# Kernel tuning notes

Measured on AMD Instinct MI355X. Metric: run time of the kernel, lower is better.

## Reference

```python
import jax, jax.numpy as jnp
import numpy as np

N_NODES = 100000
N_EDGES = 1600000
IN_SIZE = 256
HID = 64
HEADS = 2
OUT_SIZE = 16


def _gat_layer(x, W, a_l, a_r, b, src, dst, n_nodes, heads, feat):
    # x: [N, Din]; W: [Din, H*F]; a_l, a_r: [H, F]; b: [H*F]
    h = (x @ W).reshape(n_nodes, heads, feat)          # [N, H, F]
    el = jnp.sum(h * a_l, axis=-1)                     # [N, H]
    er = jnp.sum(h * a_r, axis=-1)                     # [N, H]
    e = jax.nn.leaky_relu(el[src] + er[dst], 0.2)      # [E, H]
    # segment softmax over incoming edges of each dst node
    m = jax.ops.segment_max(e, dst, num_segments=n_nodes)
    m = jnp.where(jnp.isfinite(m), m, 0.0)             # nodes with no in-edges
    p = jnp.exp(e - m[dst])                            # [E, H]
    s = jax.ops.segment_sum(p, dst, num_segments=n_nodes)
    alpha = p / (s[dst] + 1e-9)                        # [E, H]
    # scatter-add weighted source features
    out = jax.ops.segment_sum(alpha[:, :, None] * h[src], dst, num_segments=n_nodes)
    return out + b.reshape(1, heads, feat)             # [N, H, F]


def setup_inputs() -> dict:
    key = jax.random.key(0)
    ks = jax.random.split(key, 12)
    features = jax.random.normal(ks[0], (N_NODES, IN_SIZE), dtype=jnp.float32)
    src = jax.random.randint(ks[1], (N_EDGES,), 0, N_NODES, dtype=jnp.int32)
    dst = jax.random.randint(ks[2], (N_EDGES,), 0, N_NODES, dtype=jnp.int32)
    s1 = 1.0 / np.sqrt(IN_SIZE)
    s2 = 1.0 / np.sqrt(HID * HEADS)
    W1 = jax.random.normal(ks[3], (IN_SIZE, HEADS * HID), dtype=jnp.float32) * s1
    al1 = jax.random.normal(ks[4], (HEADS, HID), dtype=jnp.float32) * 0.1
    ar1 = jax.random.normal(ks[5], (HEADS, HID), dtype=jnp.float32) * 0.1
    b1 = jnp.zeros((HEADS * HID,), dtype=jnp.float32)
    W2 = jax.random.normal(ks[6], (HEADS * HID, HEADS * HID), dtype=jnp.float32) * s2
    al2 = jax.random.normal(ks[7], (HEADS, HID), dtype=jnp.float32) * 0.1
    ar2 = jax.random.normal(ks[8], (HEADS, HID), dtype=jnp.float32) * 0.1
    b2 = jnp.zeros((HEADS * HID,), dtype=jnp.float32)
    Wl = jax.random.normal(ks[9], (HEADS * HID, OUT_SIZE), dtype=jnp.float32) * s2
    bl = jnp.zeros((OUT_SIZE,), dtype=jnp.float32)
    return {"features": features, "src": src, "dst": dst,
            "W1": W1, "al1": al1, "ar1": ar1, "b1": b1,
            "W2": W2, "al2": al2, "ar2": ar2, "b2": b2,
            "Wl": Wl, "bl": bl}


def reference(features, src, dst, W1, al1, ar1, b1, W2, al2, ar2, b2, Wl, bl):
    n = features.shape[0]
    h = _gat_layer(features, W1, al1, ar1, b1.reshape(HEADS, HID).reshape(-1),
                   src, dst, n, HEADS, HID)
    h = jax.nn.elu(h.reshape(n, HEADS * HID))          # flatten(1) + ELU (dropout: eval)
    h = _gat_layer(h, W2, al2, ar2, b2, src, dst, n, HEADS, HID)
    h = jax.nn.elu(h.reshape(n, HEADS * HID))
    return h @ Wl + bl                                  # [N, OUT_SIZE]
```

## Files before the change

kernel.cpp:

```cpp
#include <hip/hip_runtime.h>
#include <hip/hip_fp16.h>

#define N_NODES 100000
#define N_EDGES 1600000
#define IN_SIZE 256
#define HID 64
#define HEADS 2
#define DMODEL 128
#define OUT_SZ 16

#define BSHIFT 9
#define BNODES 512
#define NB 196
#define CAP 16384
#define EPB 4096

typedef _Float16 f16x4 __attribute__((ext_vector_type(4)));
typedef _Float16 f16x8 __attribute__((ext_vector_type(8)));
typedef float f32x4 __attribute__((ext_vector_type(4)));


__global__ __launch_bounds__(256) void bin_kernel(const int* __restrict__ src,
                                                  const int* __restrict__ dst,
                                                  int* __restrict__ counts,
                                                  int2* __restrict__ bucketbuf, int e) {
    __shared__ int hist[NB];
    __shared__ int base[NB];
    int tid = threadIdx.x;
    int start = blockIdx.x * EPB;
    for (int i = tid; i < NB; i += 256) hist[i] = 0;
    __syncthreads();
    int pack[16];
    #pragma unroll
    for (int i = 0; i < 16; i++) {
        int idx = start + i * 256 + tid;
        int p = -1;
        if (idx < e) {
            int b = dst[idx] >> BSHIFT;
            int r = atomicAdd(&hist[b], 1);
            p = (b << 16) | r;
        }
        pack[i] = p;
    }
    __syncthreads();
    for (int i = tid; i < NB; i += 256)
        base[i] = atomicAdd(&counts[i], hist[i]);
    __syncthreads();
    #pragma unroll
    for (int i = 0; i < 16; i++) {
        int idx = start + i * 256 + tid;
        int p = pack[i];
        if (p >= 0) {
            int b = p >> 16;
            int pos = base[b] + (p & 0xffff);
            if (pos < CAP)
                bucketbuf[(size_t)b * CAP + pos] = make_int2(src[idx], dst[idx]);
        }
    }
}

__global__ void bucket_scan_kernel(const int* __restrict__ counts,
                                   int* __restrict__ bases) {
    __shared__ int lds[256];
    int tid = threadIdx.x;
    int t = (tid < NB) ? min(counts[tid], CAP) : 0;
    lds[tid] = t;
    __syncthreads();
    for (int off = 1; off < 256; off <<= 1) {
        int x = 0;
        if (tid >= off) x = lds[tid - off];
        __syncthreads();
        lds[tid] += x;
        __syncthreads();
    }
    if (tid < NB) bases[tid] = lds[tid] - t;
}


__global__ __launch_bounds__(256) void csr_kernel(const int2* __restrict__ bucketbuf,
                                                  const int* __restrict__ counts,
                                                  const int* __restrict__ bases,
                                                  int* __restrict__ deg,
                                                  int* __restrict__ offs,
                                                  int* __restrict__ ssrc, int n) {
    __shared__ int hist[BNODES];
    __shared__ int cursor[BNODES];
    __shared__ int lds[256];
    int b = blockIdx.x;
    int tid = threadIdx.x;
    int cnt = min(counts[b], CAP);
    int base = bases[b];
    int node0 = b << BSHIFT;
    const int2* ebuf = bucketbuf + (size_t)b * CAP;

    hist[tid] = 0;
    hist[tid + 256] = 0;
    __syncthreads();
    for (int i = tid; i < cnt; i += 256)
        atomicAdd(&hist[ebuf[i].y - node0], 1);
    __syncthreads();

    int h0 = hist[2 * tid], h1 = hist[2 * tid + 1];
    lds[tid] = h0 + h1;
    __syncthreads();
    for (int off = 1; off < 256; off <<= 1) {
        int x = 0;
        if (tid >= off) x = lds[tid - off];
        __syncthreads();
        lds[tid] += x;
        __syncthreads();
    }
    int excl = lds[tid] - (h0 + h1);
    cursor[2 * tid] = excl;
    cursor[2 * tid + 1] = excl + h0;
    int g0 = node0 + 2 * tid, g1 = g0 + 1;
    if (g0 < n) { deg[g0] = h0; offs[g0] = base + excl; }
    if (g1 < n) { deg[g1] = h1; offs[g1] = base + excl + h0; }
    __syncthreads();

    for (int i = tid; i < cnt; i += 256) {
        int2 ed = ebuf[i];
        int p = atomicAdd(&cursor[ed.y - node0], 1);
        ssrc[base + p] = ed.x;
    }
}


template <int K>
__global__ void wt_kernel(const float* __restrict__ W, _Float16* __restrict__ Wt) {
    int i = blockIdx.x * blockDim.x + threadIdx.x;
    if (i >= 128 * K) return;
    int nr = i / K;
    int k = i - nr * K;
    Wt[i] = (_Float16)W[(size_t)k * 128 + nr];
}


template <int K, bool F16IN>
__global__ __launch_bounds__(256) void gemm_attn_kernel(const void* __restrict__ Ap,
                                                        const _Float16* __restrict__ Wt,
                                                        const float* __restrict__ al,
                                                        const float* __restrict__ ar,
                                                        uint32_t* __restrict__ h16,
                                                        float* __restrict__ el,
                                                        float* __restrict__ er, int n) {
    __shared__ _Float16 As[64 * 72];
    __shared__ _Float16 Bs[128 * 72];
    int tid = threadIdx.x;
    int w = tid >> 6;
    int lane = tid & 63;
    int c = lane & 15;
    int quad = lane >> 4;
    int r0 = blockIdx.x * 64;

    f32x4 acc[8];
    #pragma unroll
    for (int t = 0; t < 8; t++) acc[t] = (f32x4){0.f, 0.f, 0.f, 0.f};

    for (int kt = 0; kt < K; kt += 64) {
        {
            int lr = tid >> 4;
            int lc = (tid & 15) * 4;
            #pragma unroll
            for (int q = 0; q < 4; q++) {
                int row = lr + 16 * q;
                int gr = r0 + row;
                if constexpr (F16IN) {
                    const uint32_t* Af = (const uint32_t*)Ap;
                    uint2 v = make_uint2(0u, 0u);
                    if (gr < n) v = *(const uint2*)(Af + (size_t)gr * (K / 2) + (kt + lc) / 2);
                    *(uint2*)(As + row * 72 + lc) = v;
                } else {
                    const float* Af = (const float*)Ap;
                    float4 v = make_float4(0.f, 0.f, 0.f, 0.f);
                    if (gr < n) v = *(const float4*)(Af + (size_t)gr * K + kt + lc);
                    f16x4 hv = {(_Float16)v.x, (_Float16)v.y, (_Float16)v.z, (_Float16)v.w};
                    *(f16x4*)(As + row * 72 + lc) = hv;
                }
            }
            int nr = tid >> 1;
            int kc = (tid & 1) * 32;
            const uint4* gsrc = (const uint4*)(Wt + (size_t)nr * K + kt + kc);
            uint4 v0 = gsrc[0];
            uint4 v1 = gsrc[1];
            uint4 v2 = gsrc[2];
            uint4 v3 = gsrc[3];
            *(uint4*)(Bs + nr * 72 + kc + 0)  = v0;
            *(uint4*)(Bs + nr * 72 + kc + 8)  = v1;
            *(uint4*)(Bs + nr * 72 + kc + 16) = v2;
            *(uint4*)(Bs + nr * 72 + kc + 24) = v3;
        }
        __syncthreads();

        #pragma unroll
        for (int kk = 0; kk < 64; kk += 32) {
            f16x8 a = *(const f16x8*)(As + (16 * w + c) * 72 + kk + quad * 8);
            #pragma unroll
            for (int t = 0; t < 8; t++) {
                f16x8 b = *(const f16x8*)(Bs + (16 * t + c) * 72 + kk + quad * 8);
                acc[t] = __builtin_amdgcn_mfma_f32_16x16x32_f16(a, b, acc[t], 0, 0, 0);
            }
        }
        __syncthreads();
    }

    #pragma unroll
    for (int i = 0; i < 4; i++) {
        int gr = r0 + 16 * w + quad * 4 + i;
        float el0 = 0.f, el1 = 0.f, er0 = 0.f, er1 = 0.f;
        #pragma unroll
        for (int t = 0; t < 8; t++) {
            float hv = acc[t][i];
            float alv = al[16 * t + c];
            float arv = ar[16 * t + c];
            if (t < 4) { el0 += hv * alv; er0 += hv * arv; }
            else       { el1 += hv * alv; er1 += hv * arv; }
        }
        #pragma unroll
        for (int off = 1; off < 16; off <<= 1) {
            el0 += __shfl_xor(el0, off);
            el1 += __shfl_xor(el1, off);
            er0 += __shfl_xor(er0, off);
            er1 += __shfl_xor(er1, off);
        }
        if (c == 0 && gr < n) {
            *(float2*)(el + 2 * gr) = make_float2(el0, el1);
            *(float2*)(er + 2 * gr) = make_float2(er0, er1);
        }
        #pragma unroll
        for (int t = 0; t < 8; t++) {
            float own = acc[t][i];
            float other = __shfl_xor(own, 1);
            if ((c & 1) == 0 && gr < n) {
                __half2 hh = __floats2half2_rn(own, other);
                h16[(size_t)gr * 64 + 8 * t + (c >> 1)] = *(const uint32_t*)&hh;
            }
        }
    }
}


__device__ __forceinline__ float edge_w(float2 e, float erh, int head) {
    float x = (head ? e.y : e.x) + erh;
    x = x >= 0.f ? x : 0.2f * x;
    return __expf(x);
}

__device__ __forceinline__ void acc8(uint4 u, float w, float* a) {
    union { uint4 u4; f16x8 h8; } cv;
    cv.u4 = u;
    #pragma unroll
    for (int i = 0; i < 8; i++)
        a[i] = fmaf((float)cv.h8[i], w, a[i]);
}

__global__ __launch_bounds__(256) void agg_kernel(const uint32_t* __restrict__ hb,
                                                  const int* __restrict__ ssrc,
                                                  const float* __restrict__ el,
                                                  const float* __restrict__ er,
                                                  const float* __restrict__ bias,
                                                  const int* __restrict__ offs,
                                                  const int* __restrict__ deg,
                                                  uint32_t* __restrict__ out16, int n) {
    int wid = (blockIdx.x * blockDim.x + threadIdx.x) >> 6;
    int lane = threadIdx.x & 63;
    if (wid >= n) return;
    int start = offs[wid];
    int d = deg[wid];
    int g = lane >> 4;
    int fl = lane & 15;
    int head = fl >> 3;

    float2 erv = *(const float2*)(er + 2 * wid);
    float erh = head ? erv.y : erv.x;

    const int* sp = ssrc + start;
    const float2* el2 = (const float2*)el;
    const char* hbb = (const char*)hb;
    uint32_t foff = (uint32_t)(fl << 4);

    float a[8];
    #pragma unroll
    for (int i = 0; i < 8; i++) a[i] = 0.f;
    float psum = 0.f;

    int j = 0;
    for (; j + 16 <= d; j += 16) {
        int s0 = sp[j + g];
        int s1 = sp[j + 4 + g];
        int s2 = sp[j + 8 + g];
        int s3 = sp[j + 12 + g];
        float2 e0 = el2[s0];
        uint4 u0 = *(const uint4*)(hbb + (((uint32_t)s0 << 8) + foff));
        float2 e1 = el2[s1];
        uint4 u1 = *(const uint4*)(hbb + (((uint32_t)s1 << 8) + foff));
        float2 e2 = el2[s2];
        uint4 u2 = *(const uint4*)(hbb + (((uint32_t)s2 << 8) + foff));
        float2 e3 = el2[s3];
        uint4 u3 = *(const uint4*)(hbb + (((uint32_t)s3 << 8) + foff));
        float w0 = edge_w(e0, erh, head);
        float w1 = edge_w(e1, erh, head);
        float w2 = edge_w(e2, erh, head);
        float w3 = edge_w(e3, erh, head);
        psum += (w0 + w1) + (w2 + w3);
        acc8(u0, w0, a);
        acc8(u1, w1, a);
        acc8(u2, w2, a);
        acc8(u3, w3, a);
    }
    if (j < d) {
        int last = d - 1;
        int i0 = j + g,      i1 = j + 4 + g, i2 = j + 8 + g, i3 = j + 12 + g;
        int c0 = min(i0, last), c1 = min(i1, last), c2 = min(i2, last), c3 = min(i3, last);
        int s0 = sp[c0];
        int s1 = sp[c1];
        int s2 = sp[c2];
        int s3 = sp[c3];
        float2 e0 = el2[s0];
        uint4 u0 = *(const uint4*)(hbb + (((uint32_t)s0 << 8) + foff));
        float2 e1 = el2[s1];
        uint4 u1 = *(const uint4*)(hbb + (((uint32_t)s1 << 8) + foff));
        float2 e2 = el2[s2];
        uint4 u2 = *(const uint4*)(hbb + (((uint32_t)s2 << 8) + foff));
        float2 e3 = el2[s3];
        uint4 u3 = *(const uint4*)(hbb + (((uint32_t)s3 << 8) + foff));
        float w0 = (i0 <= last) ? edge_w(e0, erh, head) : 0.f;
        float w1 = (i1 <= last) ? edge_w(e1, erh, head) : 0.f;
        float w2 = (i2 <= last) ? edge_w(e2, erh, head) : 0.f;
        float w3 = (i3 <= last) ? edge_w(e3, erh, head) : 0.f;
        psum += (w0 + w1) + (w2 + w3);
        acc8(u0, w0, a);
        acc8(u1, w1, a);
        acc8(u2, w2, a);
        acc8(u3, w3, a);
    }

    #pragma unroll
    for (int i = 0; i < 8; i++) {
        a[i] += __shfl_xor(a[i], 16);
        a[i] += __shfl_xor(a[i], 32);
    }
    psum += __shfl_xor(psum, 16);
    psum += __shfl_xor(psum, 32);

    if (lane < 16) {
        float inv = 1.f / (psum + 1e-9f);
        float4 b0 = *(const float4*)(bias + 8 * lane);
        float4 b1 = *(const float4*)(bias + 8 * lane + 4);
        float o[8];
        o[0] = fmaf(a[0], inv, b0.x);
        o[1] = fmaf(a[1], inv, b0.y);
        o[2] = fmaf(a[2], inv, b0.z);
        o[3] = fmaf(a[3], inv, b0.w);
        o[4] = fmaf(a[4], inv, b1.x);
        o[5] = fmaf(a[5], inv, b1.y);
        o[6] = fmaf(a[6], inv, b1.z);
        o[7] = fmaf(a[7], inv, b1.w);
        #pragma unroll
        for (int i = 0; i < 8; i++)
            o[i] = o[i] > 0.f ? o[i] : (__expf(o[i]) - 1.f);
        __half2 h01 = __floats2half2_rn(o[0], o[1]);
        __half2 h23 = __floats2half2_rn(o[2], o[3]);
        __half2 h45 = __floats2half2_rn(o[4], o[5]);
        __half2 h67 = __floats2half2_rn(o[6], o[7]);
        uint4 ov = make_uint4(*(const uint32_t*)&h01, *(const uint32_t*)&h23,
                              *(const uint32_t*)&h45, *(const uint32_t*)&h67);
        ((uint4*)(out16 + (size_t)wid * 64))[lane] = ov;
    }
}


__global__ __launch_bounds__(256) void final_kernel(const uint32_t* __restrict__ x16,
                                                    const float* __restrict__ Wl,
                                                    const float* __restrict__ bl,
                                                    float* __restrict__ out, int n) {
    __shared__ float Ws[DMODEL * OUT_SZ];
    __shared__ float bs[OUT_SZ];
    int tid = threadIdx.x;
    for (int i = tid; i < DMODEL * OUT_SZ / 4; i += 256)
        ((float4*)Ws)[i] = ((const float4*)Wl)[i];
    if (tid < OUT_SZ) bs[tid] = bl[tid];
    __syncthreads();
    int node = blockIdx.x * 16 + (tid >> 4);
    int c = tid & 15;
    if (node >= n) return;
    const uint2* xr = (const uint2*)(x16 + (size_t)node * 64);
    float acc = bs[c];
    #pragma unroll
    for (int kk = 0; kk < 32; kk++) {
        uint2 v = xr[kk];
        float2 f0 = __half22float2(*(const __half2*)&v.x);
        float2 f1 = __half22float2(*(const __half2*)&v.y);
        acc += f0.x * Ws[(4 * kk + 0) * OUT_SZ + c];
        acc += f0.y * Ws[(4 * kk + 1) * OUT_SZ + c];
        acc += f1.x * Ws[(4 * kk + 2) * OUT_SZ + c];
        acc += f1.y * Ws[(4 * kk + 3) * OUT_SZ + c];
    }
    out[(size_t)node * OUT_SZ + c] = acc;
}


extern "C" void kernel_launch(void* const* d_in, const int* in_sizes, int n_in,
                              void* d_out, int out_size, void* d_ws, size_t ws_size,
                              hipStream_t stream) {
    const float* features = (const float*)d_in[0];
    const int*   src      = (const int*)d_in[1];
    const int*   dst      = (const int*)d_in[2];
    const float* W1  = (const float*)d_in[3];
    const float* al1 = (const float*)d_in[4];
    const float* ar1 = (const float*)d_in[5];
    const float* b1  = (const float*)d_in[6];
    const float* W2  = (const float*)d_in[7];
    const float* al2 = (const float*)d_in[8];
    const float* ar2 = (const float*)d_in[9];
    const float* b2  = (const float*)d_in[10];
    const float* Wl  = (const float*)d_in[11];
    const float* bl  = (const float*)d_in[12];
    float* out = (float*)d_out;

    const int n = N_NODES, e = N_EDGES;

    char* w = (char*)d_ws;
    uint32_t* h16 = (uint32_t*)w;       w += (size_t)n * 64 * 4;
    uint32_t* x1  = (uint32_t*)w;       w += (size_t)n * 64 * 4;
    uint32_t* x2  = (uint32_t*)w;       w += 26 * 1024 * 1024;
    float* el   = (float*)w;            w += (size_t)n * 2 * 4;
    float* er   = (float*)w;            w += (size_t)n * 2 * 4;
    int* deg    = (int*)w;              w += 400128;
    int* offs   = (int*)w;              w += 400128;
    int* ssrc   = (int*)w;              w += (size_t)e * 4;
    int* counts = (int*)w;              w += 1024;
    int* bases  = (int*)w;              w += 1024;
    _Float16* Wt1 = (_Float16*)w;       w += 128 * IN_SIZE * 2;
    _Float16* Wt2 = (_Float16*)w;       w += 128 * DMODEL * 2;
    int2* bucketbuf = (int2*)x2;

    const int binBlocks = (e + EPB - 1) / EPB;
    const int gemmBlocks = (n + 63) / 64;
    const int nodeWaveBlocks = (n + 3) / 4;
    const int finalBlocks = (n + 15) / 16;

    hipMemsetAsync(counts, 0, NB * 4, stream);
    bin_kernel<<<binBlocks, 256, 0, stream>>>(src, dst, counts, bucketbuf, e);
    bucket_scan_kernel<<<1, 256, 0, stream>>>(counts, bases);
    csr_kernel<<<NB, 256, 0, stream>>>(bucketbuf, counts, bases, deg, offs, ssrc, n);

    wt_kernel<IN_SIZE><<<(128 * IN_SIZE + 255) / 256, 256, 0, stream>>>(W1, Wt1);
    wt_kernel<DMODEL><<<(128 * DMODEL + 255) / 256, 256, 0, stream>>>(W2, Wt2);

    gemm_attn_kernel<IN_SIZE, false><<<gemmBlocks, 256, 0, stream>>>(features, Wt1, al1, ar1,
                                                                     h16, el, er, n);
    agg_kernel<<<nodeWaveBlocks, 256, 0, stream>>>(h16, ssrc, el, er, b1, offs, deg, x1, n);

    gemm_attn_kernel<DMODEL, true><<<gemmBlocks, 256, 0, stream>>>(x1, Wt2, al2, ar2,
                                                                   h16, el, er, n);
    agg_kernel<<<nodeWaveBlocks, 256, 0, stream>>>(h16, ssrc, el, er, b2, offs, deg, x2, n);

    final_kernel<<<finalBlocks, 256, 0, stream>>>(x2, Wl, bl, out, n);

    (void)in_sizes; (void)n_in; (void)out_size; (void)ws_size;
}
```

Baseline: 434.8 us.

## Split aggregation per head across blocks, one wave per node-head pair

The aggregation kernel now launches twice as many blocks, and each wave handles a single attention head of one node instead of both heads. Within a wave, 8 lanes cover one head's 128 bytes of fp16 features, and 8 edge groups each process 2 edges per 16-edge step. The goal is more parallelism and fewer registers per wave, since each lane holds 2 outstanding gathers instead of 4. The cost is that the index list and destination metadata are read twice per node, and it needs one extra shuffle-reduction step.

```diff
diff --git a/kernel.cpp b/kernel.cpp
--- a/kernel.cpp
+++ b/kernel.cpp
@@ -240,8 +240,8 @@
 }
 
 
-__device__ __forceinline__ float edge_w(float2 e, float erh, int head) {
-    float x = (head ? e.y : e.x) + erh;
+__device__ __forceinline__ float edge_w1(float e, float erh) {
+    float x = e + erh;
     x = x >= 0.f ? x : 0.2f * x;
     return __expf(x);
 }
@@ -262,22 +262,22 @@
                                                   const int* __restrict__ offs,
                                                   const int* __restrict__ deg,
                                                   uint32_t* __restrict__ out16, int n) {
-    int wid = (blockIdx.x * blockDim.x + threadIdx.x) >> 6;
+    int b = blockIdx.x;
+    int half = b & 1;
+    int node = ((b >> 1) << 2) + (threadIdx.x >> 6);
+    if (node >= n) return;
     int lane = threadIdx.x & 63;
-    if (wid >= n) return;
-    int start = offs[wid];
-    int d = deg[wid];
-    int g = lane >> 4;
-    int fl = lane & 15;
-    int head = fl >> 3;
-
-    float2 erv = *(const float2*)(er + 2 * wid);
-    float erh = head ? erv.y : erv.x;
+    int g = lane >> 3;
+    int fl = lane & 7;
+
+    float erh = er[2 * node + half];
+    int start = offs[node];
+    int d = deg[node];
 
     const int* sp = ssrc + start;
-    const float2* el2 = (const float2*)el;
+    const float* elh = el + half;
     const char* hbb = (const char*)hb;
-    uint32_t foff = (uint32_t)(fl << 4);
+    uint32_t foff = (uint32_t)((half << 7) + (fl << 4));
 
     float a[8];
     #pragma unroll
@@ -287,66 +287,48 @@
     int j = 0;
     for (; j + 16 <= d; j += 16) {
         int s0 = sp[j + g];
-        int s1 = sp[j + 4 + g];
-        int s2 = sp[j + 8 + g];
-        int s3 = sp[j + 12 + g];
-        float2 e0 = el2[s0];
+        int s1 = sp[j + 8 + g];
+        float e0 = elh[2 * s0];
         uint4 u0 = *(const uint4*)(hbb + (((uint32_t)s0 << 8) + foff));
-        float2 e1 = el2[s1];
+        float e1 = elh[2 * s1];
         uint4 u1 = *(const uint4*)(hbb + (((uint32_t)s1 << 8) + foff));
-        float2 e2 = el2[s2];
-        uint4 u2 = *(const uint4*)(hbb + (((uint32_t)s2 << 8) + foff));
-        float2 e3 = el2[s3];
-        uint4 u3 = *(const uint4*)(hbb + (((uint32_t)s3 << 8) + foff));
-        float w0 = edge_w(e0, erh, head);
-        float w1 = edge_w(e1, erh, head);
-        float w2 = edge_w(e2, erh, head);
-        float w3 = edge_w(e3, erh, head);
-        psum += (w0 + w1) + (w2 + w3);
+        float w0 = edge_w1(e0, erh);
+        float w1 = edge_w1(e1, erh);
+        psum += w0 + w1;
         acc8(u0, w0, a);
         acc8(u1, w1, a);
-        acc8(u2, w2, a);
-        acc8(u3, w3, a);
     }
     if (j < d) {
         int last = d - 1;
-        int i0 = j + g,      i1 = j + 4 + g, i2 = j + 8 + g, i3 = j + 12 + g;
-        int c0 = min(i0, last), c1 = min(i1, last), c2 = min(i2, last), c3 = min(i3, last);
-        int s0 = sp[c0];
-        int s1 = sp[c1];
-        int s2 = sp[c2];
-        int s3 = sp[c3];
-        float2 e0 = el2[s0];
+        int i0 = j + g, i1 = j + 8 + g;
+        int s0 = sp[min(i0, last)];
+        int s1 = sp[min(i1, last)];
+        float e0 = elh[2 * s0];
         uint4 u0 = *(const uint4*)(hbb + (((uint32_t)s0 << 8) + foff));
-        float2 e1 = el2[s1];
+        float e1 = elh[2 * s1];
         uint4 u1 = *(const uint4*)(hbb + (((uint32_t)s1 << 8) + foff));
-        float2 e2 = el2[s2];
-        uint4 u2 = *(const uint4*)(hbb + (((uint32_t)s2 << 8) + foff));
-        float2 e3 = el2[s3];
-        uint4 u3 = *(const uint4*)(hbb + (((uint32_t)s3 << 8) + foff));
-        float w0 = (i0 <= last) ? edge_w(e0, erh, head) : 0.f;
-        float w1 = (i1 <= last) ? edge_w(e1, erh, head) : 0.f;
-        float w2 = (i2 <= last) ? edge_w(e2, erh, head) : 0.f;
-        float w3 = (i3 <= last) ? edge_w(e3, erh, head) : 0.f;
-        psum += (w0 + w1) + (w2 + w3);
+        float w0 = (i0 <= last) ? edge_w1(e0, erh) : 0.f;
+        float w1 = (i1 <= last) ? edge_w1(e1, erh) : 0.f;
+        psum += w0 + w1;
         acc8(u0, w0, a);
         acc8(u1, w1, a);
-        acc8(u2, w2, a);
-        acc8(u3, w3, a);
     }
 
     #pragma unroll
     for (int i = 0; i < 8; i++) {
+        a[i] += __shfl_xor(a[i], 8);
         a[i] += __shfl_xor(a[i], 16);
         a[i] += __shfl_xor(a[i], 32);
     }
+    psum += __shfl_xor(psum, 8);
     psum += __shfl_xor(psum, 16);
     psum += __shfl_xor(psum, 32);
 
-    if (lane < 16) {
+    if (lane < 8) {
         float inv = 1.f / (psum + 1e-9f);
-        float4 b0 = *(const float4*)(bias + 8 * lane);
-        float4 b1 = *(const float4*)(bias + 8 * lane + 4);
+        const float* bh = bias + (half << 6) + 8 * lane;
+        float4 b0 = *(const float4*)(bh);
+        float4 b1 = *(const float4*)(bh + 4);
         float o[8];
         o[0] = fmaf(a[0], inv, b0.x);
         o[1] = fmaf(a[1], inv, b0.y);
@@ -365,7 +347,7 @@
         __half2 h67 = __floats2half2_rn(o[6], o[7]);
         uint4 ov = make_uint4(*(const uint32_t*)&h01, *(const uint32_t*)&h23,
                               *(const uint32_t*)&h45, *(const uint32_t*)&h67);
-        ((uint4*)(out16 + (size_t)wid * 64))[lane] = ov;
+        *(uint4*)(out16 + (size_t)node * 64 + (half << 5) + 4 * lane) = ov;
     }
 }
 
@@ -437,7 +419,7 @@
 
     const int binBlocks = (e + EPB - 1) / EPB;
     const int gemmBlocks = (n + 63) / 64;
-    const int nodeWaveBlocks = (n + 3) / 4;
+    const int aggBlocks = 2 * ((n + 3) / 4);
     const int finalBlocks = (n + 15) / 16;
 
     hipMemsetAsync(counts, 0, NB * 4, stream);
@@ -450,11 +432,11 @@
 
     gemm_attn_kernel<IN_SIZE, false><<<gemmBlocks, 256, 0, stream>>>(features, Wt1, al1, ar1,
                                                                      h16, el, er, n);
-    agg_kernel<<<nodeWaveBlocks, 256, 0, stream>>>(h16, ssrc, el, er, b1, offs, deg, x1, n);
+    agg_kernel<<<aggBlocks, 256, 0, stream>>>(h16, ssrc, el, er, b1, offs, deg, x1, n);
 
     gemm_attn_kernel<DMODEL, true><<<gemmBlocks, 256, 0, stream>>>(x1, Wt2, al2, ar2,
                                                                    h16, el, er, n);
-    agg_kernel<<<nodeWaveBlocks, 256, 0, stream>>>(h16, ssrc, el, er, b2, offs, deg, x2, n);
+    agg_kernel<<<aggBlocks, 256, 0, stream>>>(h16, ssrc, el, er, b2, offs, deg, x2, n);
 
     final_kernel<<<finalBlocks, 256, 0, stream>>>(x2, Wl, bl, out, n);
 
```

Result: slower. 466.0 us (+7.2%).
